# Performance work log

Measured on AMD Instinct MI355X. Metric: run time of the kernel, lower is better.

Reference implementation:

```python
import jax, jax.numpy as jnp
import numpy as np

WINDOW_SIZE = 7
NUM_HEADS = 6
DIM = 192
HEAD_DIM = DIM // NUM_HEADS


def _relative_position_index(ws: int) -> np.ndarray:
    coords = np.stack(np.meshgrid(np.arange(ws), np.arange(ws), indexing='ij'))  # [2, ws, ws]
    coords = coords.reshape(2, -1)  # [2, ws*ws]
    rel = coords[:, :, None] - coords[:, None, :]  # [2, N, N]
    rel = rel.transpose(1, 2, 0).astype(np.int64)  # [N, N, 2]
    rel[..., 0] += ws - 1
    rel[..., 1] += ws - 1
    rel[..., 0] *= 2 * ws - 1
    return rel.sum(-1)  # [N, N] in [0, (2*ws-1)^2)


def setup_inputs() -> dict:
    key = jax.random.key(0)
    ks = jax.random.split(key, 6)
    B, N, C = 8192, WINDOW_SIZE * WINDOW_SIZE, DIM
    return {
        'x': jax.random.normal(ks[0], (B, N, C), dtype=jnp.float32),
        'qkv_w': jax.random.normal(ks[1], (3 * C, C), dtype=jnp.float32) * 0.02,
        'qkv_b': jax.random.normal(ks[2], (3 * C,), dtype=jnp.float32) * 0.02,
        'proj_w': jax.random.normal(ks[3], (C, C), dtype=jnp.float32) * 0.02,
        'proj_b': jax.random.normal(ks[4], (C,), dtype=jnp.float32) * 0.02,
        'bias_table': jax.random.normal(ks[5], ((2 * WINDOW_SIZE - 1) ** 2, NUM_HEADS), dtype=jnp.float32) * 0.02,
    }


def reference(x, qkv_w, qkv_b, proj_w, proj_b, bias_table):
    B, N, C = x.shape
    H, hd = NUM_HEADS, HEAD_DIM
    scale = hd ** -0.5
    rel_idx = jnp.asarray(_relative_position_index(WINDOW_SIZE))  # [N, N] static

    qkv = x @ qkv_w.T + qkv_b  # [B, N, 3C]
    qkv = qkv.reshape(B, N, 3, H, hd).transpose(2, 0, 3, 1, 4)  # [3, B, H, N, hd]
    q, k, v = qkv[0], qkv[1], qkv[2]

    attn = jnp.einsum('bhnd,bhmd->bhnm', q * scale, k)  # [B, H, N, N]
    bias = bias_table[rel_idx]  # [N, N, H]
    attn = attn + bias.transpose(2, 0, 1)[None]  # broadcast over B
    attn = jax.nn.softmax(attn, axis=-1)

    out = jnp.einsum('bhnm,bhmd->bhnd', attn, v)  # [B, H, N, hd]
    out = out.transpose(0, 2, 1, 3).reshape(B, N, C)
    return out @ proj_w.T + proj_b
```

## Files before the change

### kernel.cpp

```cpp
#include <hip/hip_runtime.h>
#include <hip/hip_bf16.h>
#include <cstdint>
#include <cstddef>

typedef float  f32x4 __attribute__((ext_vector_type(4)));
typedef short  s16x8 __attribute__((ext_vector_type(8)));

#define NTOK   49
#define CDIM   192
#define HEADS  6
#define SCALE  0.17677669529663689f
#define LOG2E  1.4426950408889634f
#define SCL2   (0.17677669529663689f * 1.4426950408889634f)

#define WS_BIAS_BYTES  98304
#define WS_WQ_BYTES    221184
#define WS_TOTAL_BYTES (WS_BIAS_BYTES + WS_WQ_BYTES + 73728)

static __device__ __forceinline__ ushort f2bf(float f) {
  __hip_bfloat16 h = __float2bfloat16(f);
  union { __hip_bfloat16 h; ushort u; } c; c.h = h;
  return c.u;
}

static __device__ __forceinline__ ushort4 pack4(f32x4 a) {
  union { ushort4 u; __hip_bfloat162 h[2]; } c;
  c.h[0] = __float22bfloat162_rn(make_float2(a[0], a[1]));
  c.h[1] = __float22bfloat162_rn(make_float2(a[2], a[3]));
  return c.u;
}

static __device__ __forceinline__ s16x8 pack8(f32x4 a, f32x4 b) {
  union { s16x8 v; __hip_bfloat162 h[4]; } u;
  u.h[0] = __float22bfloat162_rn(make_float2(a[0], a[1]));
  u.h[1] = __float22bfloat162_rn(make_float2(a[2], a[3]));
  u.h[2] = __float22bfloat162_rn(make_float2(b[0], b[1]));
  u.h[3] = __float22bfloat162_rn(make_float2(b[2], b[3]));
  return u.v;
}

static __device__ __forceinline__ f32x4 mfma_bf16(s16x8 a, s16x8 b, f32x4 c) {
  return __builtin_amdgcn_mfma_f32_16x16x32_bf16(a, b, c, 0, 0, 0);
}

__global__ void wconv_kernel(const float* __restrict__ qkv_w,
                             const float* __restrict__ proj_w,
                             const float* __restrict__ bias_table,
                             ushort* __restrict__ wqs, ushort* __restrict__ wps,
                             float* __restrict__ biasT) {
  int i = blockIdx.x * 256 + threadIdx.x;
  if (i < 576 * 192) {
    int n = i / 192, k = i % 192;
    int dst = ((n >> 4) * 6 + (k >> 5)) * 512 + ((k >> 3) & 3) * 128 + (n & 15) * 8 + (k & 7);
    wqs[dst] = f2bf(qkv_w[i]);
  }
  if (i < 192 * 192) {
    int n = i / 192, k = i % 192;
    int dst = ((n >> 4) * 6 + (k >> 5)) * 512 + ((k >> 3) & 3) * 128 + (n & 15) * 8 + (k & 7);
    wps[dst] = f2bf(proj_w[i]);
  }
  if (i < HEADS * 4096) {
    int h = i >> 12, r = i & 4095;
    int lane = (r >> 2) & 63, e = r & 3;
    int qt = r >> 10, kt = (r >> 8) & 3;
    int q   = qt * 16 + (lane & 15);
    int key = kt * 16 + (lane >> 4) * 4 + e;
    float v;
    if (key >= NTOK)      v = -1e30f;
    else if (q >= NTOK)   v = 0.f;
    else {
      int qd = q / 7, qm = q % 7, kd = key / 7, km = key % 7;
      int ri = (qd - kd + 6) * 13 + (qm - km + 6);
      v = bias_table[ri * 6 + h] * LOG2E;
    }
    biasT[i] = v;
  }
}

template <bool WB>
__global__ __launch_bounds__(768, 3)
void wattn_kernel(const float* __restrict__ x,
                  const float* __restrict__ qkv_w, const float* __restrict__ qkv_b,
                  const float* __restrict__ proj_w, const float* __restrict__ proj_b,
                  const float* __restrict__ bias_table,
                  const ushort* __restrict__ wqs, const ushort* __restrict__ wps,
                  const float* __restrict__ biasT,
                  float* __restrict__ out, int nwin) {
  __shared__ __align__(16) ushort XB[2][64 * 200];
  __shared__ __align__(16) float  BL[WB ? 4 : 1024];

  const int tid  = threadIdx.x;
  const int lane = tid & 63;
  const int wv   = tid >> 6;
  const int winl = wv / 6;
  const int w    = wv - winl * 6;
  const int l16  = lane & 15;
  const int lk   = lane >> 4;
  const int win  = blockIdx.x * 2 + winl;
  const int h    = w;

#pragma unroll
  for (int it = 0; it < 8; ++it) {
    int v = tid + it * 768;
    int wl2 = v / 3072, r = v - wl2 * 3072;
    int row = r / 48, c4 = r - row * 48;
    int wgl = blockIdx.x * 2 + wl2;
    float4 f = {0.f, 0.f, 0.f, 0.f};
    if (row < NTOK && wgl < nwin)
      f = *(const float4*)(x + (size_t)wgl * (NTOK * CDIM) + row * CDIM + c4 * 4);
    union { ushort4 u; __hip_bfloat162 h[2]; } cc;
    cc.h[0] = __float22bfloat162_rn(make_float2(f.x, f.y));
    cc.h[1] = __float22bfloat162_rn(make_float2(f.z, f.w));
    *(ushort4*)&XB[wl2][row * 200 + c4 * 4] = cc.u;
  }
  if constexpr (!WB) {
    for (int v = tid; v < 169 * 6; v += 768) BL[v] = bias_table[v];
  }
  __syncthreads();

  s16x8 bq[4], ak[4], bv[2][2];

  {
    f32x4 qacc[2][4] = {};
    f32x4 kacc[2][4] = {};
#pragma unroll
    for (int ks = 0; ks < 6; ++ks) {
      const int k0 = ks * 32 + lk * 8;
      s16x8 xa[4];
#pragma unroll
      for (int mt = 0; mt < 4; ++mt)
        xa[mt] = *(const s16x8*)&XB[winl][(mt * 16 + l16) * 200 + k0];
#pragma unroll
      for (int nt2 = 0; nt2 < 2; ++nt2) {
        s16x8 wqf, wkf;
        if constexpr (WB) {
          const int lo = lk * 128 + l16 * 8;
          wqf = *(const s16x8*)&wqs[(((0 * 12 + w * 2 + nt2) * 6 + ks) << 9) + lo];
          wkf = *(const s16x8*)&wqs[(((1 * 12 + w * 2 + nt2) * 6 + ks) << 9) + lo];
        } else {
          const int nq = w * 32 + nt2 * 16 + l16;
          const float* pp;
          pp = qkv_w + (0 * 192 + nq) * 192 + k0;
          { float4 f0 = *(const float4*)pp, f1 = *(const float4*)(pp + 4);
            f32x4 a = {f0.x,f0.y,f0.z,f0.w}, b = {f1.x,f1.y,f1.z,f1.w}; wqf = pack8(a, b); }
          pp = qkv_w + (1 * 192 + nq) * 192 + k0;
          { float4 f0 = *(const float4*)pp, f1 = *(const float4*)(pp + 4);
            f32x4 a = {f0.x,f0.y,f0.z,f0.w}, b = {f1.x,f1.y,f1.z,f1.w}; wkf = pack8(a, b); }
        }
#pragma unroll
        for (int mt = 0; mt < 4; ++mt) {
          qacc[nt2][mt] = mfma_bf16(wqf, xa[mt], qacc[nt2][mt]);
          kacc[nt2][mt] = mfma_bf16(wkf, xa[mt], kacc[nt2][mt]);
        }
      }
    }
    {
      const float4 b0 = *(const float4*)&qkv_b[0 * 192 + w * 32 +  0 + lk * 4];
      const float4 b1 = *(const float4*)&qkv_b[0 * 192 + w * 32 + 16 + lk * 4];
#pragma unroll
      for (int t = 0; t < 4; ++t) {
        f32x4 a0 = qacc[0][t], a1 = qacc[1][t];
        a0[0]=(a0[0]+b0.x)*SCL2; a0[1]=(a0[1]+b0.y)*SCL2; a0[2]=(a0[2]+b0.z)*SCL2; a0[3]=(a0[3]+b0.w)*SCL2;
        a1[0]=(a1[0]+b1.x)*SCL2; a1[1]=(a1[1]+b1.y)*SCL2; a1[2]=(a1[2]+b1.z)*SCL2; a1[3]=(a1[3]+b1.w)*SCL2;
        bq[t] = pack8(a0, a1);
      }
    }
#pragma unroll
    for (int t = 0; t < 4; ++t)
      ak[t] = pack8(kacc[0][t], kacc[1][t]);
  }

  {
    f32x4 vacc[4][2] = {};
#pragma unroll
    for (int ks = 0; ks < 6; ++ks) {
      const int k0 = ks * 32 + lk * 8;
      s16x8 xa[4];
#pragma unroll
      for (int mt = 0; mt < 4; ++mt)
        xa[mt] = *(const s16x8*)&XB[winl][(mt * 16 + l16) * 200 + k0];
#pragma unroll
      for (int nt2 = 0; nt2 < 2; ++nt2) {
        s16x8 wf;
        if constexpr (WB) {
          wf = *(const s16x8*)&wqs[(((2 * 12 + w * 2 + nt2) * 6 + ks) << 9) + lk * 128 + l16 * 8];
        } else {
          const float* pp = qkv_w + (2 * 192 + w * 32 + nt2 * 16 + l16) * 192 + k0;
          float4 f0 = *(const float4*)pp, f1 = *(const float4*)(pp + 4);
          f32x4 a = {f0.x,f0.y,f0.z,f0.w}, b = {f1.x,f1.y,f1.z,f1.w}; wf = pack8(a, b);
        }
#pragma unroll
        for (int mt = 0; mt < 4; ++mt)
          vacc[mt][nt2] = mfma_bf16(xa[mt], wf, vacc[mt][nt2]);
      }
    }
#pragma unroll
    for (int nd = 0; nd < 2; ++nd) {
      const float vb = qkv_b[2 * 192 + w * 32 + nd * 16 + l16];
      f32x4 v0 = vacc[0][nd], v1 = vacc[1][nd], v2 = vacc[2][nd], v3 = vacc[3][nd];
#pragma unroll
      for (int i = 0; i < 4; ++i) { v0[i]+=vb; v1[i]+=vb; v2[i]+=vb; v3[i]+=vb; }
      bv[nd][0] = pack8(v0, v1);
      bv[nd][1] = pack8(v2, v3);
    }
  }
  __syncthreads();

  ushort* xbw = XB[winl];
#pragma unroll
  for (int qt = 0; qt < 4; ++qt) {
    f32x4 s[4];
#pragma unroll
    for (int kt = 0; kt < 4; ++kt) {
      f32x4 z = {0.f, 0.f, 0.f, 0.f};
      s[kt] = mfma_bf16(ak[kt], bq[qt], z);
    }
    float mx = -1e30f;
    if constexpr (WB) {
#pragma unroll
      for (int kt = 0; kt < 4; ++kt) {
        f32x4 b4 = *(const f32x4*)&biasT[h * 4096 + qt * 1024 + kt * 256 + lane * 4];
#pragma unroll
        for (int i = 0; i < 4; ++i) {
          float sv = s[kt][i] + b4[i];
          s[kt][i] = sv;
          mx = fmaxf(mx, sv);
        }
      }
    } else {
      const int q  = qt * 16 + l16;
      const int qd = q / 7, qm = q % 7;
#pragma unroll
      for (int kt = 0; kt < 4; ++kt)
#pragma unroll
        for (int i = 0; i < 4; ++i) {
          const int key = kt * 16 + lk * 4 + i;
          float sv = s[kt][i];
          if (key < NTOK) {
            int kd = key / 7, km = key % 7;
            int ri = (qd - kd + 6) * 13 + (qm - km + 6);
            ri = ri < 0 ? 0 : (ri > 168 ? 168 : ri);
            sv += BL[ri * 6 + h] * LOG2E;
          } else sv = -1e30f;
          s[kt][i] = sv;
          mx = fmaxf(mx, sv);
        }
    }
    mx = fmaxf(mx, __shfl_xor(mx, 16));
    mx = fmaxf(mx, __shfl_xor(mx, 32));
    float sum = 0.f;
#pragma unroll
    for (int kt = 0; kt < 4; ++kt)
#pragma unroll
      for (int i = 0; i < 4; ++i) {
        float pv = exp2f(s[kt][i] - mx);
        s[kt][i] = pv; sum += pv;
      }
    sum += __shfl_xor(sum, 16);
    sum += __shfl_xor(sum, 32);
    const float rinv = 1.f / sum;

    s16x8 pa0 = pack8(s[0], s[1]);
    s16x8 pa1 = pack8(s[2], s[3]);
#pragma unroll
    for (int nd = 0; nd < 2; ++nd) {
      f32x4 z = {0.f, 0.f, 0.f, 0.f};
      f32x4 o = mfma_bf16(bv[nd][0], pa0, z);
      o = mfma_bf16(bv[nd][1], pa1, o);
      o[0] *= rinv; o[1] *= rinv; o[2] *= rinv; o[3] *= rinv;
      *(ushort4*)&xbw[(qt * 16 + l16) * 200 + h * 32 + nd * 16 + lk * 4] = pack4(o);
    }
  }
  __syncthreads();

  {
    f32x4 pc[2][4] = {};
#pragma unroll
    for (int ks = 0; ks < 6; ++ks) {
      const int k0 = ks * 32 + lk * 8;
      s16x8 a[4];
#pragma unroll
      for (int mt = 0; mt < 4; ++mt)
        a[mt] = *(const s16x8*)&XB[winl][(mt * 16 + l16) * 200 + k0];
#pragma unroll
      for (int nt = 0; nt < 2; ++nt) {
        s16x8 b;
        if constexpr (WB) {
          b = *(const s16x8*)&wps[(((w * 2 + nt) * 6 + ks) << 9) + lk * 128 + l16 * 8];
        } else {
          const int n = w * 32 + nt * 16 + l16;
          const float* pp = proj_w + n * 192 + k0;
          float4 f0 = *(const float4*)pp, f1 = *(const float4*)(pp + 4);
          f32x4 fa = {f0.x,f0.y,f0.z,f0.w}, fb = {f1.x,f1.y,f1.z,f1.w};
          b = pack8(fa, fb);
        }
#pragma unroll
        for (int mt = 0; mt < 4; ++mt)
          pc[nt][mt] = mfma_bf16(b, a[mt], pc[nt][mt]);
      }
    }
    if (win < nwin) {
#pragma unroll
      for (int nt = 0; nt < 2; ++nt) {
        const float4 pb4 = *(const float4*)&proj_b[w * 32 + nt * 16 + lk * 4];
#pragma unroll
        for (int mt = 0; mt < 4; ++mt) {
          const int row = mt * 16 + l16;
          if (row < NTOK) {
            f32x4 o = pc[nt][mt];
            o[0] += pb4.x; o[1] += pb4.y; o[2] += pb4.z; o[3] += pb4.w;
            *(float4*)&out[((size_t)win * NTOK + row) * CDIM + w * 32 + nt * 16 + lk * 4] =
                make_float4(o[0], o[1], o[2], o[3]);
          }
        }
      }
    }
  }
}

extern "C" void kernel_launch(void* const* d_in, const int* in_sizes, int n_in,
                              void* d_out, int out_size, void* d_ws, size_t ws_size,
                              hipStream_t stream) {
  const float* x          = (const float*)d_in[0];
  const float* qkv_w      = (const float*)d_in[1];
  const float* qkv_b      = (const float*)d_in[2];
  const float* proj_w     = (const float*)d_in[3];
  const float* proj_b     = (const float*)d_in[4];
  const float* bias_table = (const float*)d_in[5];
  float* out = (float*)d_out;

  const int nwin = in_sizes[0] / (NTOK * CDIM);
  const int nblk = (nwin + 1) / 2;

  if (ws_size >= WS_TOTAL_BYTES) {
    float*  biasT = (float*)d_ws;
    ushort* wqs   = (ushort*)((char*)d_ws + WS_BIAS_BYTES);
    ushort* wps   = (ushort*)((char*)d_ws + WS_BIAS_BYTES + WS_WQ_BYTES);
    wconv_kernel<<<dim3(432), dim3(256), 0, stream>>>(qkv_w, proj_w, bias_table, wqs, wps, biasT);
    wattn_kernel<true><<<dim3(nblk), dim3(768), 0, stream>>>(
        x, qkv_w, qkv_b, proj_w, proj_b, bias_table, wqs, wps, biasT, out, nwin);
  } else {
    wattn_kernel<false><<<dim3(nblk), dim3(768), 0, stream>>>(
        x, qkv_w, qkv_b, proj_w, proj_b, bias_table, nullptr, nullptr, nullptr, out, nwin);
  }
}
```

Measured before the change: 420.7 us.

## Process four window pairs per block and prefetch next pair via async global-to-LDS loads

Each block now loops over four window pairs instead of one. The next pair's fp32 input is prefetched into a new ~74KB LDS staging buffer with global_load_lds while the current pair computes, so global load latency overlaps with MFMA work. The extra LDS roughly doubles per-block shared memory, which likely cuts the number of resident blocks per CU below the launch_bounds target of 3. It also makes the grid four times smaller, lowering parallel slack and leaving a tail imbalance.

```diff
diff --git a/kernel.cpp b/kernel.cpp
--- a/kernel.cpp
+++ b/kernel.cpp
@@ -12,6 +12,7 @@
 #define SCALE  0.17677669529663689f
 #define LOG2E  1.4426950408889634f
 #define SCL2   (0.17677669529663689f * 1.4426950408889634f)
+#define PPB    4
 
 #define WS_BIAS_BYTES  98304
 #define WS_WQ_BYTES    221184
@@ -86,6 +87,7 @@
                   const ushort* __restrict__ wqs, const ushort* __restrict__ wps,
                   const float* __restrict__ biasT,
                   float* __restrict__ out, int nwin) {
+  __shared__ __align__(16) float  XF[WB ? 18944 : 4];
   __shared__ __align__(16) ushort XB[2][64 * 200];
   __shared__ __align__(16) float  BL[WB ? 4 : 1024];
 
@@ -96,65 +98,118 @@
   const int w    = wv - winl * 6;
   const int l16  = lane & 15;
   const int lk   = lane >> 4;
-  const int win  = blockIdx.x * 2 + winl;
   const int h    = w;
 
-#pragma unroll
-  for (int it = 0; it < 8; ++it) {
-    int v = tid + it * 768;
-    int wl2 = v / 3072, r = v - wl2 * 3072;
-    int row = r / 48, c4 = r - row * 48;
-    int wgl = blockIdx.x * 2 + wl2;
-    float4 f = {0.f, 0.f, 0.f, 0.f};
-    if (row < NTOK && wgl < nwin)
-      f = *(const float4*)(x + (size_t)wgl * (NTOK * CDIM) + row * CDIM + c4 * 4);
-    union { ushort4 u; __hip_bfloat162 h[2]; } cc;
-    cc.h[0] = __float22bfloat162_rn(make_float2(f.x, f.y));
-    cc.h[1] = __float22bfloat162_rn(make_float2(f.z, f.w));
-    *(ushort4*)&XB[wl2][row * 200 + c4 * 4] = cc.u;
-  }
-  if constexpr (!WB) {
+  const int npairs = (nwin + 1) / 2;
+  const int pair0  = blockIdx.x * PPB;
+  const float* xlast = x + (size_t)nwin * (NTOK * CDIM) - 4;
+
+  auto stage_issue = [&](int pidx) {
+    const float* srcp = x + (size_t)pidx * (2 * NTOK * CDIM);
+    for (int c = wv; c < 74; c += 12) {
+      const float* g = srcp + c * 256 + lane * 4;
+      if (g > xlast) g = xlast;
+      __builtin_amdgcn_global_load_lds(
+          (const __attribute__((address_space(1))) void*)g,
+          (__attribute__((address_space(3))) void*)&XF[c * 256], 16, 0, 0);
+    }
+  };
+
+  if constexpr (WB) {
+    stage_issue(pair0);
+  } else {
     for (int v = tid; v < 169 * 6; v += 768) BL[v] = bias_table[v];
   }
-  __syncthreads();
-
-  s16x8 bq[4], ak[4], bv[2][2];
-
-  {
-    f32x4 qacc[2][4] = {};
-    f32x4 kacc[2][4] = {};
-#pragma unroll
-    for (int ks = 0; ks < 6; ++ks) {
-      const int k0 = ks * 32 + lk * 8;
-      s16x8 xa[4];
-#pragma unroll
-      for (int mt = 0; mt < 4; ++mt)
-        xa[mt] = *(const s16x8*)&XB[winl][(mt * 16 + l16) * 200 + k0];
-#pragma unroll
-      for (int nt2 = 0; nt2 < 2; ++nt2) {
-        s16x8 wqf, wkf;
-        if constexpr (WB) {
-          const int lo = lk * 128 + l16 * 8;
-          wqf = *(const s16x8*)&wqs[(((0 * 12 + w * 2 + nt2) * 6 + ks) << 9) + lo];
-          wkf = *(const s16x8*)&wqs[(((1 * 12 + w * 2 + nt2) * 6 + ks) << 9) + lo];
-        } else {
-          const int nq = w * 32 + nt2 * 16 + l16;
-          const float* pp;
-          pp = qkv_w + (0 * 192 + nq) * 192 + k0;
-          { float4 f0 = *(const float4*)pp, f1 = *(const float4*)(pp + 4);
-            f32x4 a = {f0.x,f0.y,f0.z,f0.w}, b = {f1.x,f1.y,f1.z,f1.w}; wqf = pack8(a, b); }
-          pp = qkv_w + (1 * 192 + nq) * 192 + k0;
-          { float4 f0 = *(const float4*)pp, f1 = *(const float4*)(pp + 4);
-            f32x4 a = {f0.x,f0.y,f0.z,f0.w}, b = {f1.x,f1.y,f1.z,f1.w}; wkf = pack8(a, b); }
-        }
-#pragma unroll
-        for (int mt = 0; mt < 4; ++mt) {
-          qacc[nt2][mt] = mfma_bf16(wqf, xa[mt], qacc[nt2][mt]);
-          kacc[nt2][mt] = mfma_bf16(wkf, xa[mt], kacc[nt2][mt]);
-        }
-      }
-    }
+
+  for (int p = 0; p < PPB; ++p) {
+    const int pairIdx = pair0 + p;
+    if (pairIdx >= npairs) break;
+    const int win = pairIdx * 2 + winl;
+
+    __syncthreads();
+
+    if constexpr (WB) {
+#pragma unroll
+      for (int it = 0; it < 7; ++it) {
+        int v = tid + it * 768;
+        if (v < 4704) {
+          int wl2 = v / 2352, r = v - wl2 * 2352;
+          int row = r / 48, c4 = r - row * 48;
+          float4 f = *(const float4*)&XF[v * 4];
+          union { ushort4 u; __hip_bfloat162 h2[2]; } cc;
+          cc.h2[0] = __float22bfloat162_rn(make_float2(f.x, f.y));
+          cc.h2[1] = __float22bfloat162_rn(make_float2(f.z, f.w));
+          *(ushort4*)&XB[wl2][row * 200 + c4 * 4] = cc.u;
+        }
+      }
+#pragma unroll
+      for (int it = 0; it < 2; ++it) {
+        int u = tid + it * 768;
+        if (u < 1440) {
+          int wl2 = u / 720, r = u - wl2 * 720;
+          int row = 49 + r / 48, c4 = r % 48;
+          ushort4 z4 = {0, 0, 0, 0};
+          *(ushort4*)&XB[wl2][row * 200 + c4 * 4] = z4;
+        }
+      }
+    } else {
+#pragma unroll
+      for (int it = 0; it < 8; ++it) {
+        int v = tid + it * 768;
+        int wl2 = v / 3072, r = v - wl2 * 3072;
+        int row = r / 48, c4 = r - row * 48;
+        int wgl = pairIdx * 2 + wl2;
+        float4 f = {0.f, 0.f, 0.f, 0.f};
+        if (row < NTOK && wgl < nwin)
+          f = *(const float4*)(x + (size_t)wgl * (NTOK * CDIM) + row * CDIM + c4 * 4);
+        union { ushort4 u; __hip_bfloat162 h2[2]; } cc;
+        cc.h2[0] = __float22bfloat162_rn(make_float2(f.x, f.y));
+        cc.h2[1] = __float22bfloat162_rn(make_float2(f.z, f.w));
+        *(ushort4*)&XB[wl2][row * 200 + c4 * 4] = cc.u;
+      }
+    }
+    __syncthreads();
+
+    if constexpr (WB) {
+      if (p + 1 < PPB && pairIdx + 1 < npairs) stage_issue(pairIdx + 1);
+    }
+
+    s16x8 bq[4], ak[4], bv[2][2];
+
     {
+      f32x4 qacc[2][4] = {};
+      f32x4 kacc[2][4] = {};
+#pragma unroll
+      for (int ks = 0; ks < 6; ++ks) {
+        const int k0 = ks * 32 + lk * 8;
+        s16x8 xa[4];
+#pragma unroll
+        for (int mt = 0; mt < 4; ++mt)
+          xa[mt] = *(const s16x8*)&XB[winl][(mt * 16 + l16) * 200 + k0];
+#pragma unroll
+        for (int nt2 = 0; nt2 < 2; ++nt2) {
+          s16x8 wqf, wkf;
+          if constexpr (WB) {
+            const int lo = lk * 128 + l16 * 8;
+            wqf = *(const s16x8*)&wqs[(((0 * 12 + w * 2 + nt2) * 6 + ks) << 9) + lo];
+            wkf = *(const s16x8*)&wqs[(((1 * 12 + w * 2 + nt2) * 6 + ks) << 9) + lo];
+          } else {
+            const int nq = w * 32 + nt2 * 16 + l16;
+            const float* pp;
+            pp = qkv_w + (0 * 192 + nq) * 192 + k0;
+            { float4 f0 = *(const float4*)pp, f1 = *(const float4*)(pp + 4);
+              f32x4 a = {f0.x,f0.y,f0.z,f0.w}, b = {f1.x,f1.y,f1.z,f1.w}; wqf = pack8(a, b); }
+            pp = qkv_w + (1 * 192 + nq) * 192 + k0;
+            { float4 f0 = *(const float4*)pp, f1 = *(const float4*)(pp + 4);
+              f32x4 a = {f0.x,f0.y,f0.z,f0.w}, b = {f1.x,f1.y,f1.z,f1.w}; wkf = pack8(a, b); }
+          }
+#pragma unroll
+          for (int mt = 0; mt < 4; ++mt) {
+            qacc[nt2][mt] = mfma_bf16(wqf, xa[mt], qacc[nt2][mt]);
+            kacc[nt2][mt] = mfma_bf16(wkf, xa[mt], kacc[nt2][mt]);
+          }
+        }
+      }
       const float4 b0 = *(const float4*)&qkv_b[0 * 192 + w * 32 +  0 + lk * 4];
       const float4 b1 = *(const float4*)&qkv_b[0 * 192 + w * 32 + 16 + lk * 4];
 #pragma unroll
@@ -164,153 +219,153 @@
         a1[0]=(a1[0]+b1.x)*SCL2; a1[1]=(a1[1]+b1.y)*SCL2; a1[2]=(a1[2]+b1.z)*SCL2; a1[3]=(a1[3]+b1.w)*SCL2;
         bq[t] = pack8(a0, a1);
       }
-    }
-#pragma unroll
-    for (int t = 0; t < 4; ++t)
-      ak[t] = pack8(kacc[0][t], kacc[1][t]);
-  }
-
-  {
-    f32x4 vacc[4][2] = {};
-#pragma unroll
-    for (int ks = 0; ks < 6; ++ks) {
-      const int k0 = ks * 32 + lk * 8;
-      s16x8 xa[4];
-#pragma unroll
-      for (int mt = 0; mt < 4; ++mt)
-        xa[mt] = *(const s16x8*)&XB[winl][(mt * 16 + l16) * 200 + k0];
-#pragma unroll
-      for (int nt2 = 0; nt2 < 2; ++nt2) {
-        s16x8 wf;
-        if constexpr (WB) {
-          wf = *(const s16x8*)&wqs[(((2 * 12 + w * 2 + nt2) * 6 + ks) << 9) + lk * 128 + l16 * 8];
-        } else {
-          const float* pp = qkv_w + (2 * 192 + w * 32 + nt2 * 16 + l16) * 192 + k0;
-          float4 f0 = *(const float4*)pp, f1 = *(const float4*)(pp + 4);
-          f32x4 a = {f0.x,f0.y,f0.z,f0.w}, b = {f1.x,f1.y,f1.z,f1.w}; wf = pack8(a, b);
-        }
+#pragma unroll
+      for (int t = 0; t < 4; ++t)
+        ak[t] = pack8(kacc[0][t], kacc[1][t]);
+    }
+
+    {
+      f32x4 vacc[4][2] = {};
+#pragma unroll
+      for (int ks = 0; ks < 6; ++ks) {
+        const int k0 = ks * 32 + lk * 8;
+        s16x8 xa[4];
 #pragma unroll
         for (int mt = 0; mt < 4; ++mt)
-          vacc[mt][nt2] = mfma_bf16(xa[mt], wf, vacc[mt][nt2]);
-      }
-    }
-#pragma unroll
-    for (int nd = 0; nd < 2; ++nd) {
-      const float vb = qkv_b[2 * 192 + w * 32 + nd * 16 + l16];
-      f32x4 v0 = vacc[0][nd], v1 = vacc[1][nd], v2 = vacc[2][nd], v3 = vacc[3][nd];
-#pragma unroll
-      for (int i = 0; i < 4; ++i) { v0[i]+=vb; v1[i]+=vb; v2[i]+=vb; v3[i]+=vb; }
-      bv[nd][0] = pack8(v0, v1);
-      bv[nd][1] = pack8(v2, v3);
-    }
-  }
-  __syncthreads();
-
-  ushort* xbw = XB[winl];
-#pragma unroll
-  for (int qt = 0; qt < 4; ++qt) {
-    f32x4 s[4];
-#pragma unroll
-    for (int kt = 0; kt < 4; ++kt) {
-      f32x4 z = {0.f, 0.f, 0.f, 0.f};
-      s[kt] = mfma_bf16(ak[kt], bq[qt], z);
-    }
-    float mx = -1e30f;
-    if constexpr (WB) {
+          xa[mt] = *(const s16x8*)&XB[winl][(mt * 16 + l16) * 200 + k0];
+#pragma unroll
+        for (int nt2 = 0; nt2 < 2; ++nt2) {
+          s16x8 wf;
+          if constexpr (WB) {
+            wf = *(const s16x8*)&wqs[(((2 * 12 + w * 2 + nt2) * 6 + ks) << 9) + lk * 128 + l16 * 8];
+          } else {
+            const float* pp = qkv_w + (2 * 192 + w * 32 + nt2 * 16 + l16) * 192 + k0;
+            float4 f0 = *(const float4*)pp, f1 = *(const float4*)(pp + 4);
+            f32x4 a = {f0.x,f0.y,f0.z,f0.w}, b = {f1.x,f1.y,f1.z,f1.w}; wf = pack8(a, b);
+          }
+#pragma unroll
+          for (int mt = 0; mt < 4; ++mt)
+            vacc[mt][nt2] = mfma_bf16(xa[mt], wf, vacc[mt][nt2]);
+        }
+      }
+#pragma unroll
+      for (int nd = 0; nd < 2; ++nd) {
+        const float vb = qkv_b[2 * 192 + w * 32 + nd * 16 + l16];
+        f32x4 v0 = vacc[0][nd], v1 = vacc[1][nd], v2 = vacc[2][nd], v3 = vacc[3][nd];
+#pragma unroll
+        for (int i = 0; i < 4; ++i) { v0[i]+=vb; v1[i]+=vb; v2[i]+=vb; v3[i]+=vb; }
+        bv[nd][0] = pack8(v0, v1);
+        bv[nd][1] = pack8(v2, v3);
+      }
+    }
+    __syncthreads();
+
+    ushort* xbw = XB[winl];
+#pragma unroll
+    for (int qt = 0; qt < 4; ++qt) {
+      f32x4 s[4];
 #pragma unroll
       for (int kt = 0; kt < 4; ++kt) {
-        f32x4 b4 = *(const f32x4*)&biasT[h * 4096 + qt * 1024 + kt * 256 + lane * 4];
+        f32x4 z = {0.f, 0.f, 0.f, 0.f};
+        s[kt] = mfma_bf16(ak[kt], bq[qt], z);
+      }
+      float mx = -1e30f;
+      if constexpr (WB) {
+#pragma unroll
+        for (int kt = 0; kt < 4; ++kt) {
+          f32x4 b4 = *(const f32x4*)&biasT[h * 4096 + qt * 1024 + kt * 256 + lane * 4];
+#pragma unroll
+          for (int i = 0; i < 4; ++i) {
+            float sv = s[kt][i] + b4[i];
+            s[kt][i] = sv;
+            mx = fmaxf(mx, sv);
+          }
+        }
+      } else {
+        const int q  = qt * 16 + l16;
+        const int qd = q / 7, qm = q % 7;
+#pragma unroll
+        for (int kt = 0; kt < 4; ++kt)
+#pragma unroll
+          for (int i = 0; i < 4; ++i) {
+            const int key = kt * 16 + lk * 4 + i;
+            float sv = s[kt][i];
+            if (key < NTOK) {
+              int kd = key / 7, km = key % 7;
+              int ri = (qd - kd + 6) * 13 + (qm - km + 6);
+              ri = ri < 0 ? 0 : (ri > 168 ? 168 : ri);
+              sv += BL[ri * 6 + h] * LOG2E;
+            } else sv = -1e30f;
+            s[kt][i] = sv;
+            mx = fmaxf(mx, sv);
+          }
+      }
+      mx = fmaxf(mx, __shfl_xor(mx, 16));
+      mx = fmaxf(mx, __shfl_xor(mx, 32));
+      float sum = 0.f;
+#pragma unroll
+      for (int kt = 0; kt < 4; ++kt)
 #pragma unroll
         for (int i = 0; i < 4; ++i) {
-          float sv = s[kt][i] + b4[i];
-          s[kt][i] = sv;
-          mx = fmaxf(mx, sv);
-        }
-      }
-    } else {
-      const int q  = qt * 16 + l16;
-      const int qd = q / 7, qm = q % 7;
-#pragma unroll
-      for (int kt = 0; kt < 4; ++kt)
-#pragma unroll
-        for (int i = 0; i < 4; ++i) {
-          const int key = kt * 16 + lk * 4 + i;
-          float sv = s[kt][i];
-          if (key < NTOK) {
-            int kd = key / 7, km = key % 7;
-            int ri = (qd - kd + 6) * 13 + (qm - km + 6);
-            ri = ri < 0 ? 0 : (ri > 168 ? 168 : ri);
-            sv += BL[ri * 6 + h] * LOG2E;
-          } else sv = -1e30f;
-          s[kt][i] = sv;
-          mx = fmaxf(mx, sv);
-        }
-    }
-    mx = fmaxf(mx, __shfl_xor(mx, 16));
-    mx = fmaxf(mx, __shfl_xor(mx, 32));
-    float sum = 0.f;
-#pragma unroll
-    for (int kt = 0; kt < 4; ++kt)
-#pragma unroll
-      for (int i = 0; i < 4; ++i) {
-        float pv = exp2f(s[kt][i] - mx);
-        s[kt][i] = pv; sum += pv;
-      }
-    sum += __shfl_xor(sum, 16);
-    sum += __shfl_xor(sum, 32);
-    const float rinv = 1.f / sum;
-
-    s16x8 pa0 = pack8(s[0], s[1]);
-    s16x8 pa1 = pack8(s[2], s[3]);
-#pragma unroll
-    for (int nd = 0; nd < 2; ++nd) {
-      f32x4 z = {0.f, 0.f, 0.f, 0.f};
-      f32x4 o = mfma_bf16(bv[nd][0], pa0, z);
-      o = mfma_bf16(bv[nd][1], pa1, o);
-      o[0] *= rinv; o[1] *= rinv; o[2] *= rinv; o[3] *= rinv;
-      *(ushort4*)&xbw[(qt * 16 + l16) * 200 + h * 32 + nd * 16 + lk * 4] = pack4(o);
-    }
-  }
-  __syncthreads();
-
-  {
-    f32x4 pc[2][4] = {};
-#pragma unroll
-    for (int ks = 0; ks < 6; ++ks) {
-      const int k0 = ks * 32 + lk * 8;
-      s16x8 a[4];
-#pragma unroll
-      for (int mt = 0; mt < 4; ++mt)
-        a[mt] = *(const s16x8*)&XB[winl][(mt * 16 + l16) * 200 + k0];
-#pragma unroll
-      for (int nt = 0; nt < 2; ++nt) {
-        s16x8 b;
-        if constexpr (WB) {
-          b = *(const s16x8*)&wps[(((w * 2 + nt) * 6 + ks) << 9) + lk * 128 + l16 * 8];
-        } else {
-          const int n = w * 32 + nt * 16 + l16;
-          const float* pp = proj_w + n * 192 + k0;
-          float4 f0 = *(const float4*)pp, f1 = *(const float4*)(pp + 4);
-          f32x4 fa = {f0.x,f0.y,f0.z,f0.w}, fb = {f1.x,f1.y,f1.z,f1.w};
-          b = pack8(fa, fb);
-        }
+          float pv = exp2f(s[kt][i] - mx);
+          s[kt][i] = pv; sum += pv;
+        }
+      sum += __shfl_xor(sum, 16);
+      sum += __shfl_xor(sum, 32);
+      const float rinv = 1.f / sum;
+
+      s16x8 pa0 = pack8(s[0], s[1]);
+      s16x8 pa1 = pack8(s[2], s[3]);
+#pragma unroll
+      for (int nd = 0; nd < 2; ++nd) {
+        f32x4 z = {0.f, 0.f, 0.f, 0.f};
+        f32x4 o = mfma_bf16(bv[nd][0], pa0, z);
+        o = mfma_bf16(bv[nd][1], pa1, o);
+        o[0] *= rinv; o[1] *= rinv; o[2] *= rinv; o[3] *= rinv;
+        *(ushort4*)&xbw[(qt * 16 + l16) * 200 + h * 32 + nd * 16 + lk * 4] = pack4(o);
+      }
+    }
+    __syncthreads();
+
+    {
+      f32x4 pc[2][4] = {};
+#pragma unroll
+      for (int ks = 0; ks < 6; ++ks) {
+        const int k0 = ks * 32 + lk * 8;
+        s16x8 a[4];
 #pragma unroll
         for (int mt = 0; mt < 4; ++mt)
-          pc[nt][mt] = mfma_bf16(b, a[mt], pc[nt][mt]);
-      }
-    }
-    if (win < nwin) {
-#pragma unroll
-      for (int nt = 0; nt < 2; ++nt) {
-        const float4 pb4 = *(const float4*)&proj_b[w * 32 + nt * 16 + lk * 4];
-#pragma unroll
-        for (int mt = 0; mt < 4; ++mt) {
-          const int row = mt * 16 + l16;
-          if (row < NTOK) {
-            f32x4 o = pc[nt][mt];
-            o[0] += pb4.x; o[1] += pb4.y; o[2] += pb4.z; o[3] += pb4.w;
-            *(float4*)&out[((size_t)win * NTOK + row) * CDIM + w * 32 + nt * 16 + lk * 4] =
-                make_float4(o[0], o[1], o[2], o[3]);
+          a[mt] = *(const s16x8*)&XB[winl][(mt * 16 + l16) * 200 + k0];
+#pragma unroll
+        for (int nt = 0; nt < 2; ++nt) {
+          s16x8 b;
+          if constexpr (WB) {
+            b = *(const s16x8*)&wps[(((w * 2 + nt) * 6 + ks) << 9) + lk * 128 + l16 * 8];
+          } else {
+            const int n = w * 32 + nt * 16 + l16;
+            const float* pp = proj_w + n * 192 + k0;
+            float4 f0 = *(const float4*)pp, f1 = *(const float4*)(pp + 4);
+            f32x4 fa = {f0.x,f0.y,f0.z,f0.w}, fb = {f1.x,f1.y,f1.z,f1.w};
+            b = pack8(fa, fb);
+          }
+#pragma unroll
+          for (int mt = 0; mt < 4; ++mt)
+            pc[nt][mt] = mfma_bf16(b, a[mt], pc[nt][mt]);
+        }
+      }
+      if (win < nwin) {
+#pragma unroll
+        for (int nt = 0; nt < 2; ++nt) {
+          const float4 pb4 = *(const float4*)&proj_b[w * 32 + nt * 16 + lk * 4];
+#pragma unroll
+          for (int mt = 0; mt < 4; ++mt) {
+            const int row = mt * 16 + l16;
+            if (row < NTOK) {
+              f32x4 o = pc[nt][mt];
+              o[0] += pb4.x; o[1] += pb4.y; o[2] += pb4.z; o[3] += pb4.w;
+              *(float4*)&out[((size_t)win * NTOK + row) * CDIM + w * 32 + nt * 16 + lk * 4] =
+                  make_float4(o[0], o[1], o[2], o[3]);
+            }
           }
         }
       }
@@ -329,8 +384,9 @@
   const float* bias_table = (const float*)d_in[5];
   float* out = (float*)d_out;
 
-  const int nwin = in_sizes[0] / (NTOK * CDIM);
-  const int nblk = (nwin + 1) / 2;
+  const int nwin   = in_sizes[0] / (NTOK * CDIM);
+  const int npairs = (nwin + 1) / 2;
+  const int nblk   = (npairs + PPB - 1) / PPB;
 
   if (ws_size >= WS_TOTAL_BYTES) {
     float*  biasT = (float*)d_ws;
```

New measurement: 746.0 us. 77.3% more time.
